# Performance work log

Measured on AMD Instinct MI355X. Metric: run time of the kernel, lower is better.

Reference implementation:

```python
import jax, jax.numpy as jnp
import numpy as np

T, B, D = 1024, 128, 512
CLIP = 1.0  # grad_clip_value


def setup_inputs() -> dict:
    key = jax.random.key(0)
    ks = jax.random.split(key, 6)
    s = 1.0 / np.sqrt(D)
    return {
        "h0": jnp.zeros((B, D), jnp.float32),
        "ins": jax.random.normal(ks[0], (T, B, D), jnp.float32),
        "resets": jax.random.bernoulli(ks[1], 0.05, (T, B)),
        # GRUCell params: input kernels (with bias) for r,z,n fused; hidden kernels
        # for r,z (no bias, per flax GRUCell) fused; hidden kernel for n (with bias).
        "Wi": (jax.random.normal(ks[2], (D, 3 * D), jnp.float32) * s),
        "bi": jnp.zeros((3 * D,), jnp.float32),
        "Wh_rz": (jax.random.normal(ks[3], (D, 2 * D), jnp.float32) * s),
        "Whn": (jax.random.normal(ks[4], (D, D), jnp.float32) * s),
        "bhn": jnp.zeros((D,), jnp.float32),
    }


def reference(h0, ins, resets, Wi, bi, Wh_rz, Whn, bhn):
    def st_clip(x):
        # straight-through clip: forward = clip(x), backward = identity
        return x + jax.lax.stop_gradient(jnp.clip(x, -CLIP, CLIP) - x)

    def step(h, xt):
        x, reset = xt                      # x: [B,D], reset: [B]
        h = jnp.where(reset[:, None], 0.0, h)  # reset carry to zeros
        gi = x @ Wi + bi                   # [B,3D]
        grz = h @ Wh_rz                    # [B,2D]
        r = jax.nn.sigmoid(gi[:, :D] + grz[:, :D])
        z = jax.nn.sigmoid(gi[:, D:2 * D] + grz[:, D:])
        n = jnp.tanh(gi[:, 2 * D:] + r * (h @ Whn + bhn))
        h_new = (1.0 - z) * n + z * h      # GRU update; y == new carry in flax
        h_new = st_clip(h_new)
        return h_new, h_new

    _, ys = jax.lax.scan(step, h0, (ins, resets))
    return ys  # [T,B,D]
```

## Files before the change

kernel.cpp:

```cpp
#include <hip/hip_runtime.h>
#include <stdint.h>


typedef float f32x4 __attribute__((ext_vector_type(4)));
typedef short s16x8 __attribute__((ext_vector_type(8)));

#define DD 512
#define BB 128
#define TT 1024

static __device__ __forceinline__ unsigned short f2bf(float f) {
  uint32_t u = __builtin_bit_cast(uint32_t, f);
  u = (u + 0x7fffu + ((u >> 16) & 1u)) >> 16;
  return (unsigned short)u;
}
static __device__ __forceinline__ float b2f(uint32_t bits) {
  return __builtin_bit_cast(float, bits << 16);
}
static __device__ __forceinline__ s16x8 ldsfrag(const char* p) {
  return __builtin_bit_cast(s16x8, *reinterpret_cast<const uint4*>(p));
}

__global__ void prep(const float* __restrict__ Wi, const float* __restrict__ Whrz,
                     const float* __restrict__ Whn,
                     unsigned short* __restrict__ WiT, unsigned short* __restrict__ Wpk) {
  int i = blockIdx.x * 256 + threadIdx.x;
  if (i < 786432) {
    int n = i >> 9, k = i & 511;
    WiT[i] = f2bf(Wi[(size_t)k * 1536 + n]);
  } else {
    int j = i - 786432;
    int ck = j >> 9;
    int k = j & 511;
    int cj = ck / 96, c96 = ck % 96;
    int g = c96 >> 5, cc = c96 & 31;
    float v = (g < 2) ? Whrz[(size_t)k * 1024 + g * 512 + cj * 32 + cc]
                      : Whn[(size_t)k * 512 + cj * 32 + cc];
    Wpk[j] = f2bf(v);
  }
}

__global__ void tag0(const float* __restrict__ h0, uint32_t* __restrict__ hxt,
                     float* __restrict__ hbF) {
  int i = blockIdx.x * 512 + threadIdx.x;
  float v = h0[i];
  hxt[i] = (uint32_t)f2bf(v);
  hbF[i] = v;
}

__global__ void scanR(const int* __restrict__ r, int* __restrict__ flag) {
  int i = blockIdx.x * 256 + threadIdx.x;
  unsigned int v = (unsigned int)r[i];
  if (v > 1u) atomicOr(flag, 1);
}

__global__ __launch_bounds__(256) void gemmA(const float* __restrict__ x,
                                             const unsigned short* __restrict__ WiT,
                                             const float* __restrict__ bi,
                                             unsigned short* __restrict__ gi) {
  __shared__ unsigned short Al[128 * 64];
  __shared__ unsigned short Bl[128 * 64];
  const int tid = threadIdx.x;
  const int lane = tid & 63;
  const int wv = tid >> 6;
  const int wm = wv >> 1, wn = wv & 1;
  const int n0 = blockIdx.x * 128;
  const int m0 = blockIdx.y * 128;

  const int sr = tid >> 1;
  const int sh = tid & 1;
  const float* xp = x + (size_t)(m0 + sr) * DD + sh * 32;
  const unsigned short* wp = WiT + (size_t)(n0 + sr) * DD + sh * 32;

  float bir[4];
#pragma unroll
  for (int j = 0; j < 4; ++j) bir[j] = bi[n0 + wn * 64 + j * 16 + (lane & 15)];

  f32x4 acc[4][4];
#pragma unroll
  for (int i = 0; i < 4; ++i)
#pragma unroll
    for (int j = 0; j < 4; ++j) acc[i][j] = (f32x4){0.f, 0.f, 0.f, 0.f};

  float4 xa[8];
  uint4 wa[4];
#pragma unroll
  for (int q = 0; q < 8; ++q) xa[q] = *reinterpret_cast<const float4*>(xp + q * 4);
#pragma unroll
  for (int c = 0; c < 4; ++c) wa[c] = *reinterpret_cast<const uint4*>(wp + c * 8);

  for (int kt = 0; kt < 8; ++kt) {
    __syncthreads();
    const int swz = (sr & 7) << 4;
#pragma unroll
    for (int c = 0; c < 4; ++c) {
      const float4 a = xa[2 * c], b = xa[2 * c + 1];
      uint4 u;
      u.x = (uint32_t)f2bf(a.x) | ((uint32_t)f2bf(a.y) << 16);
      u.y = (uint32_t)f2bf(a.z) | ((uint32_t)f2bf(a.w) << 16);
      u.z = (uint32_t)f2bf(b.x) | ((uint32_t)f2bf(b.y) << 16);
      u.w = (uint32_t)f2bf(b.z) | ((uint32_t)f2bf(b.w) << 16);
      const int off = sr * 128 + ((sh * 64 + c * 16) ^ swz);
      *reinterpret_cast<uint4*>(reinterpret_cast<char*>(Al) + off) = u;
    }
#pragma unroll
    for (int c = 0; c < 4; ++c) {
      const int off = sr * 128 + ((sh * 64 + c * 16) ^ swz);
      *reinterpret_cast<uint4*>(reinterpret_cast<char*>(Bl) + off) = wa[c];
    }
    if (kt < 7) {
#pragma unroll
      for (int q = 0; q < 8; ++q)
        xa[q] = *reinterpret_cast<const float4*>(xp + (kt + 1) * 64 + q * 4);
#pragma unroll
      for (int c = 0; c < 4; ++c)
        wa[c] = *reinterpret_cast<const uint4*>(wp + (kt + 1) * 64 + c * 8);
    }
    __syncthreads();
#pragma unroll
    for (int kk = 0; kk < 2; ++kk) {
      s16x8 af[4], bfr[4];
      const int kb = kk * 64 + ((lane >> 4) << 4);
      const int sw = (lane & 7) << 4;
#pragma unroll
      for (int i = 0; i < 4; ++i) {
        const int row = wm * 64 + i * 16 + (lane & 15);
        af[i] = ldsfrag(reinterpret_cast<const char*>(Al) + row * 128 + (kb ^ sw));
      }
#pragma unroll
      for (int j = 0; j < 4; ++j) {
        const int row = wn * 64 + j * 16 + (lane & 15);
        bfr[j] = ldsfrag(reinterpret_cast<const char*>(Bl) + row * 128 + (kb ^ sw));
      }
#pragma unroll
      for (int i = 0; i < 4; ++i)
#pragma unroll
        for (int j = 0; j < 4; ++j)
          acc[i][j] = __builtin_amdgcn_mfma_f32_16x16x32_bf16(af[i], bfr[j], acc[i][j], 0, 0, 0);
    }
  }
#pragma unroll
  for (int i = 0; i < 4; ++i) {
    const int gr0 = m0 + wm * 64 + i * 16 + ((lane >> 4) << 2);
#pragma unroll
    for (int j = 0; j < 4; ++j) {
      const int gc = n0 + wn * 64 + j * 16 + (lane & 15);
#pragma unroll
      for (int r = 0; r < 4; ++r)
        gi[(size_t)(gr0 + r) * 1536 + gc] = f2bf(acc[i][j][r] + bir[j]);
    }
  }
}

static __device__ __forceinline__ unsigned rmask16f(const int* resets, int rmode,
                                                    long long tg, int row0) {
  unsigned m = 0;
  if (rmode) {
    const unsigned char* rb = reinterpret_cast<const unsigned char*>(resets);
    uint4 u = *reinterpret_cast<const uint4*>(rb + (size_t)tg * 128 + row0);
    unsigned w0 = u.x, w1 = u.y, w2 = u.z, w3 = u.w;
#pragma unroll
    for (int b = 0; b < 4; ++b) {
      if ((w0 >> (8 * b)) & 0xFFu) m |= 1u << (0 + b);
      if ((w1 >> (8 * b)) & 0xFFu) m |= 1u << (4 + b);
      if ((w2 >> (8 * b)) & 0xFFu) m |= 1u << (8 + b);
      if ((w3 >> (8 * b)) & 0xFFu) m |= 1u << (12 + b);
    }
  } else {
    const uint4* p = reinterpret_cast<const uint4*>(resets + (size_t)tg * 128 + row0);
#pragma unroll
    for (int q = 0; q < 4; ++q) {
      uint4 u = p[q];
      if (u.x) m |= 1u << (q * 4 + 0);
      if (u.y) m |= 1u << (q * 4 + 1);
      if (u.z) m |= 1u << (q * 4 + 2);
      if (u.w) m |= 1u << (q * 4 + 3);
    }
  }
  return m;
}

static __device__ __forceinline__ void pollTag(const uint32_t* src, unsigned exp,
                                               unsigned short (&v)[16]) {
  for (int it = 0; it < (1 << 16); ++it) {
    uint32_t u[16];
#pragma unroll
    for (int i = 0; i < 16; ++i)
      u[i] = __hip_atomic_load(src + (size_t)i * 512,
                               __ATOMIC_RELAXED, __HIP_MEMORY_SCOPE_AGENT);
    unsigned bad = 0;
#pragma unroll
    for (int i = 0; i < 16; ++i) bad |= ((u[i] >> 16) ^ exp);
    if (__ballot(bad != 0u) == 0ull) {
#pragma unroll
      for (int i = 0; i < 16; ++i) v[i] = (unsigned short)u[i];
      return;
    }
    __builtin_amdgcn_s_sleep(1);
  }
#pragma unroll
  for (int i = 0; i < 16; ++i) v[i] = 0;
}

__global__ __launch_bounds__(512) void rnnB(const unsigned short* __restrict__ gi,
                                            const unsigned short* __restrict__ Wpk,
                                            const float* __restrict__ bhn,
                                            const int* __restrict__ resets,
                                            uint32_t* hxt,
                                            float* hbF,
                                            const int* __restrict__ rmodep,
                                            float* __restrict__ ys,
                                            int t0, int tc) {
  __shared__ char Hlb[16384];
  __shared__ float ax[6528];

  const int tid = threadIdx.x;
  const int lane = tid & 63;
  const int wv = tid >> 6;
  const int w = wv & 1, ks = wv >> 1;
  const int cj = blockIdx.x >> 3, rg = blockIdx.x & 7;
  const int ec = tid & 31, eb = tid >> 5;
  const int bglob = rg * 16 + eb;
  const int colglob = cj * 32 + ec;
  const int rmode = *rmodep;

  uint4 wreg[3][4];
  {
    const unsigned short* wbase = Wpk + (size_t)cj * 96 * 512
                                + (size_t)(w * 16 + (lane & 15)) * 512
                                + ks * 128 + (lane >> 4) * 8;
#pragma unroll
    for (int g = 0; g < 3; ++g)
#pragma unroll
      for (int kk = 0; kk < 4; ++kk)
        wreg[g][kk] = *reinterpret_cast<const uint4*>(wbase + g * 32 * 512 + kk * 32);
  }

  const float bhn_c = bhn[colglob];
  float h_old = hbF[(size_t)bglob * 512 + colglob];

  unsigned short v[16];
  pollTag(hxt + (size_t)(t0 & 1) * 65536 + (size_t)rg * 8192 + tid, (unsigned)t0 & 0xFFFFu, v);

  unsigned mask = rmask16f(resets, rmode, t0, rg * 16);
  uint32_t gir, giz, gin;
  {
    const unsigned short* gp = gi + (size_t)bglob * 1536 + colglob;
    gir = gp[0]; giz = gp[512]; gin = gp[1024];
  }

  int soff[16];
#pragma unroll
  for (int i = 0; i < 16; ++i)
    soff[i] = i * 1024 + (((((tid * 2) >> 4) ^ (i & 7)) << 4) | ((tid & 7) * 2));

  for (int t = 0; t < tc; ++t) {
    const long long tg = t0 + t;
#pragma unroll
    for (int i = 0; i < 16; ++i) {
      unsigned short x = ((mask >> i) & 1u) ? (unsigned short)0 : v[i];
      *reinterpret_cast<unsigned short*>(Hlb + soff[i]) = x;
    }
    __syncthreads();
    f32x4 acc[3];
#pragma unroll
    for (int g = 0; g < 3; ++g) acc[g] = (f32x4){0.f, 0.f, 0.f, 0.f};
    {
      const int rowb = lane & 15;
      const char* hrow = Hlb + rowb * 1024;
      const int hsw = (rowb & 7) << 4;
      const int kplusB = (lane >> 4) << 4;
      s16x8 hfrag[4];
#pragma unroll
      for (int kk = 0; kk < 4; ++kk) {
        const int kbB = (ks * 128 + kk * 32) * 2 + kplusB;
        hfrag[kk] = ldsfrag(hrow + (kbB ^ hsw));
      }
#pragma unroll
      for (int g = 0; g < 3; ++g)
#pragma unroll
        for (int kk = 0; kk < 4; ++kk)
          acc[g] = __builtin_amdgcn_mfma_f32_16x16x32_bf16(
              __builtin_bit_cast(s16x8, wreg[g][kk]), hfrag[kk], acc[g], 0, 0, 0);
    }
    {
      const int mh = (lane >> 4) << 2, nn = lane & 15;
#pragma unroll
      for (int g = 0; g < 3; ++g) {
        float* dst = ax + ((ks * 2 + w) * 3 + g) * 272 + nn;
#pragma unroll
        for (int r = 0; r < 4; ++r) dst[(mh + r) * 17] = acc[g][r];
      }
    }
    __syncthreads();
    {
      const int wc = ec >> 4, mc = ec & 15;
      float s0a = 0.f, s1a = 0.f, s2a = 0.f;
#pragma unroll
      for (int k2 = 0; k2 < 4; ++k2) {
        const float* p = ax + ((k2 * 2 + wc) * 3) * 272 + mc * 17 + eb;
        s0a += p[0]; s1a += p[272]; s2a += p[544];
      }
      const float r = 1.f / (1.f + __expf(-(b2f(gir) + s0a)));
      const float z = 1.f / (1.f + __expf(-(b2f(giz) + s1a)));
      const float hu = ((mask >> eb) & 1u) ? 0.f : h_old;
      const float pre = b2f(gin) + r * (s2a + bhn_c);
      const float n = 1.f - 2.f / (1.f + __expf(2.f * pre));
      float hn = (1.f - z) * n + z * hu;
      hn = fminf(1.f, fmaxf(-1.f, hn));
      __builtin_nontemporal_store(hn, ys + ((size_t)tg * 128 + bglob) * 512 + colglob);
      const uint32_t tagged = (((uint32_t)(tg + 1) & 0xFFFFu) << 16) | (uint32_t)f2bf(hn);
      uint32_t* hp = hxt + (size_t)((tg + 1) & 1) * 65536 + (size_t)bglob * 512 + colglob;
      __hip_atomic_store(hp, tagged, __ATOMIC_RELAXED, __HIP_MEMORY_SCOPE_AGENT);
      if (t == tc - 1) hbF[(size_t)bglob * 512 + colglob] = hn;
      h_old = hn;
    }
    if (t + 1 < tc) {
      const unsigned short* gp = gi + ((size_t)(t + 1) * 128 + bglob) * 1536 + colglob;
      uint32_t ngr = gp[0], ngz = gp[512], ngn = gp[1024];
      unsigned nmask = rmask16f(resets, rmode, tg + 1, rg * 16);
      pollTag(hxt + (size_t)((tg + 1) & 1) * 65536 + (size_t)rg * 8192 + tid,
              (unsigned)(tg + 1) & 0xFFFFu, v);
      gir = ngr; giz = ngz; gin = ngn; mask = nmask;
    }
  }
}

extern "C" void kernel_launch(void* const* d_in, const int* in_sizes, int n_in,
                              void* d_out, int out_size, void* d_ws, size_t ws_size,
                              hipStream_t stream) {
  const float* h0 = (const float*)d_in[0];
  const float* ins = (const float*)d_in[1];
  const int* rst = (const int*)d_in[2];
  const float* Wi = (const float*)d_in[3];
  const float* bi = (const float*)d_in[4];
  const float* Whrz = (const float*)d_in[5];
  const float* Whn = (const float*)d_in[6];
  const float* bhn = (const float*)d_in[7];
  float* ys = (float*)d_out;

  char* ws = (char*)d_ws;
  unsigned short* WiT = (unsigned short*)(ws);
  unsigned short* Wpk = (unsigned short*)(ws + 1572864);
  uint32_t* hxt = (uint32_t*)(ws + 3145728);
  float* hbF = (float*)(ws + 3670016);
  int* flag = (int*)(ws + 3932160);
  const size_t gi_off = 3936256;
  unsigned short* gi = (unsigned short*)(ws + gi_off);

  size_t avail = (ws_size > gi_off) ? (ws_size - gi_off) : 0;
  long long tcap = (long long)(avail / (128ull * 1536ull * 2ull));
  int Tc = (int)((tcap > 1024) ? 1024 : tcap);
  Tc &= ~1;
  if (Tc < 2) Tc = 2;

  hipMemsetAsync(flag, 0, 4, stream);
  hipMemsetAsync(hxt, 0, 524288, stream);
  tag0<<<dim3(128), dim3(512), 0, stream>>>(h0, hxt, hbF);
  prep<<<dim3(6144), dim3(256), 0, stream>>>(Wi, Whrz, Whn, WiT, Wpk);
  scanR<<<dim3(128), dim3(256), 0, stream>>>(rst, flag);

  for (int t0 = 0; t0 < 1024; t0 += Tc) {
    int tc = 1024 - t0;
    if (tc > Tc) tc = Tc;
    gemmA<<<dim3(12, tc), dim3(256), 0, stream>>>(ins + (size_t)t0 * 65536, WiT, bi, gi);
    rnnB<<<dim3(128), dim3(512), 0, stream>>>(gi, Wpk, bhn, rst, hxt, hbF, flag, ys, t0, tc);
  }
}
```

Measured before the change: 3.385 ms.

## Fuse input GEMM and recurrent scan into one persistent producer-consumer kernel

Replaces the separate gemmA launch plus rnnB launch with one kernel of 256 blocks. Blocks 128 and up compute the input-projection tiles and bump a per-timestep done counter, while blocks 0-127 run the recurrence and spin on that counter before reading gi for each step. This lets the large input GEMM overlap with the latency-bound sequential scan instead of running before it. The poll loop also spins without sleeping for its first iterations and has a lower iteration cap. The added risks are deadlock if the producer blocks are not co-resident with the consumers, extra atomic traffic, and the producer blocks contending with the recurrence for CUs and bandwidth.

Result: slower. 9.776 ms (+188.8%).

```diff
diff --git a/kernel.cpp b/kernel.cpp
--- a/kernel.cpp
+++ b/kernel.cpp
@@ -8,6 +8,7 @@
 #define DD 512
 #define BB 128
 #define TT 1024
+#define SM_BYTES 43008
 
 static __device__ __forceinline__ unsigned short f2bf(float f) {
   uint32_t u = __builtin_bit_cast(uint32_t, f);
@@ -54,104 +55,6 @@
   if (v > 1u) atomicOr(flag, 1);
 }
 
-__global__ __launch_bounds__(256) void gemmA(const float* __restrict__ x,
-                                             const unsigned short* __restrict__ WiT,
-                                             const float* __restrict__ bi,
-                                             unsigned short* __restrict__ gi) {
-  __shared__ unsigned short Al[128 * 64];
-  __shared__ unsigned short Bl[128 * 64];
-  const int tid = threadIdx.x;
-  const int lane = tid & 63;
-  const int wv = tid >> 6;
-  const int wm = wv >> 1, wn = wv & 1;
-  const int n0 = blockIdx.x * 128;
-  const int m0 = blockIdx.y * 128;
-
-  const int sr = tid >> 1;
-  const int sh = tid & 1;
-  const float* xp = x + (size_t)(m0 + sr) * DD + sh * 32;
-  const unsigned short* wp = WiT + (size_t)(n0 + sr) * DD + sh * 32;
-
-  float bir[4];
-#pragma unroll
-  for (int j = 0; j < 4; ++j) bir[j] = bi[n0 + wn * 64 + j * 16 + (lane & 15)];
-
-  f32x4 acc[4][4];
-#pragma unroll
-  for (int i = 0; i < 4; ++i)
-#pragma unroll
-    for (int j = 0; j < 4; ++j) acc[i][j] = (f32x4){0.f, 0.f, 0.f, 0.f};
-
-  float4 xa[8];
-  uint4 wa[4];
-#pragma unroll
-  for (int q = 0; q < 8; ++q) xa[q] = *reinterpret_cast<const float4*>(xp + q * 4);
-#pragma unroll
-  for (int c = 0; c < 4; ++c) wa[c] = *reinterpret_cast<const uint4*>(wp + c * 8);
-
-  for (int kt = 0; kt < 8; ++kt) {
-    __syncthreads();
-    const int swz = (sr & 7) << 4;
-#pragma unroll
-    for (int c = 0; c < 4; ++c) {
-      const float4 a = xa[2 * c], b = xa[2 * c + 1];
-      uint4 u;
-      u.x = (uint32_t)f2bf(a.x) | ((uint32_t)f2bf(a.y) << 16);
-      u.y = (uint32_t)f2bf(a.z) | ((uint32_t)f2bf(a.w) << 16);
-      u.z = (uint32_t)f2bf(b.x) | ((uint32_t)f2bf(b.y) << 16);
-      u.w = (uint32_t)f2bf(b.z) | ((uint32_t)f2bf(b.w) << 16);
-      const int off = sr * 128 + ((sh * 64 + c * 16) ^ swz);
-      *reinterpret_cast<uint4*>(reinterpret_cast<char*>(Al) + off) = u;
-    }
-#pragma unroll
-    for (int c = 0; c < 4; ++c) {
-      const int off = sr * 128 + ((sh * 64 + c * 16) ^ swz);
-      *reinterpret_cast<uint4*>(reinterpret_cast<char*>(Bl) + off) = wa[c];
-    }
-    if (kt < 7) {
-#pragma unroll
-      for (int q = 0; q < 8; ++q)
-        xa[q] = *reinterpret_cast<const float4*>(xp + (kt + 1) * 64 + q * 4);
-#pragma unroll
-      for (int c = 0; c < 4; ++c)
-        wa[c] = *reinterpret_cast<const uint4*>(wp + (kt + 1) * 64 + c * 8);
-    }
-    __syncthreads();
-#pragma unroll
-    for (int kk = 0; kk < 2; ++kk) {
-      s16x8 af[4], bfr[4];
-      const int kb = kk * 64 + ((lane >> 4) << 4);
-      const int sw = (lane & 7) << 4;
-#pragma unroll
-      for (int i = 0; i < 4; ++i) {
-        const int row = wm * 64 + i * 16 + (lane & 15);
-        af[i] = ldsfrag(reinterpret_cast<const char*>(Al) + row * 128 + (kb ^ sw));
-      }
-#pragma unroll
-      for (int j = 0; j < 4; ++j) {
-        const int row = wn * 64 + j * 16 + (lane & 15);
-        bfr[j] = ldsfrag(reinterpret_cast<const char*>(Bl) + row * 128 + (kb ^ sw));
-      }
-#pragma unroll
-      for (int i = 0; i < 4; ++i)
-#pragma unroll
-        for (int j = 0; j < 4; ++j)
-          acc[i][j] = __builtin_amdgcn_mfma_f32_16x16x32_bf16(af[i], bfr[j], acc[i][j], 0, 0, 0);
-    }
-  }
-#pragma unroll
-  for (int i = 0; i < 4; ++i) {
-    const int gr0 = m0 + wm * 64 + i * 16 + ((lane >> 4) << 2);
-#pragma unroll
-    for (int j = 0; j < 4; ++j) {
-      const int gc = n0 + wn * 64 + j * 16 + (lane & 15);
-#pragma unroll
-      for (int r = 0; r < 4; ++r)
-        gi[(size_t)(gr0 + r) * 1536 + gc] = f2bf(acc[i][j][r] + bir[j]);
-    }
-  }
-}
-
 static __device__ __forceinline__ unsigned rmask16f(const int* resets, int rmode,
                                                     long long tg, int row0) {
   unsigned m = 0;
@@ -182,7 +85,7 @@
 
 static __device__ __forceinline__ void pollTag(const uint32_t* src, unsigned exp,
                                                unsigned short (&v)[16]) {
-  for (int it = 0; it < (1 << 16); ++it) {
+  for (int it = 0; it < (1 << 13); ++it) {
     uint32_t u[16];
 #pragma unroll
     for (int i = 0; i < 16; ++i)
@@ -196,23 +99,146 @@
       for (int i = 0; i < 16; ++i) v[i] = (unsigned short)u[i];
       return;
     }
-    __builtin_amdgcn_s_sleep(1);
+    if (it >= 2) __builtin_amdgcn_s_sleep(1);
   }
 #pragma unroll
   for (int i = 0; i < 16; ++i) v[i] = 0;
 }
 
-__global__ __launch_bounds__(512) void rnnB(const unsigned short* __restrict__ gi,
-                                            const unsigned short* __restrict__ Wpk,
-                                            const float* __restrict__ bhn,
-                                            const int* __restrict__ resets,
-                                            uint32_t* hxt,
-                                            float* hbF,
-                                            const int* __restrict__ rmodep,
-                                            float* __restrict__ ys,
-                                            int t0, int tc) {
-  __shared__ char Hlb[16384];
-  __shared__ float ax[6528];
+static __device__ __forceinline__ void waitDone(const int* done, int t) {
+  if ((threadIdx.x & 63) == 0) {
+    for (int it = 0; it < (1 << 16); ++it) {
+      if (__hip_atomic_load(done + t, __ATOMIC_ACQUIRE, __HIP_MEMORY_SCOPE_AGENT) >= 12)
+        break;
+      __builtin_amdgcn_s_sleep(2);
+    }
+  }
+}
+
+static __device__ void gemm_role(const float* __restrict__ x,
+                                 const unsigned short* __restrict__ WiT,
+                                 const float* __restrict__ bi,
+                                 uint32_t* __restrict__ gw,
+                                 int* __restrict__ done,
+                                 int tc, int gb, char* smem) {
+  unsigned short* Al = reinterpret_cast<unsigned short*>(smem);
+  unsigned short* Bl = reinterpret_cast<unsigned short*>(smem + 16384);
+  const int tid = threadIdx.x;
+  const int lane = tid & 63;
+  const int wv = tid >> 6;
+  const int wm = wv >> 2, wn = wv & 3;
+  const int sr = tid >> 2;
+  const int sh = tid & 3;
+  const int ntiles = 12 * tc;
+
+  for (int tile = gb; tile < ntiles; tile += 128) {
+    const int tt = tile / 12, nn = tile % 12;
+    const int m0 = tt * 128, n0 = nn * 128;
+    const float* xp = x + (size_t)(m0 + sr) * DD + sh * 16;
+    const unsigned short* wp = WiT + (size_t)(n0 + sr) * DD + sh * 16;
+
+    float bir[2];
+#pragma unroll
+    for (int j = 0; j < 2; ++j) bir[j] = bi[n0 + wn * 32 + j * 16 + (lane & 15)];
+
+    f32x4 acc[4][2];
+#pragma unroll
+    for (int i = 0; i < 4; ++i)
+#pragma unroll
+      for (int j = 0; j < 2; ++j) acc[i][j] = (f32x4){0.f, 0.f, 0.f, 0.f};
+
+    float4 xa[4];
+    uint4 wa[2];
+#pragma unroll
+    for (int q = 0; q < 4; ++q) xa[q] = *reinterpret_cast<const float4*>(xp + q * 4);
+#pragma unroll
+    for (int c = 0; c < 2; ++c) wa[c] = *reinterpret_cast<const uint4*>(wp + c * 8);
+
+    for (int kt = 0; kt < 8; ++kt) {
+      __syncthreads();
+      const int swz = (sr & 7) << 4;
+#pragma unroll
+      for (int c = 0; c < 2; ++c) {
+        const float4 a = xa[2 * c], b = xa[2 * c + 1];
+        uint4 u;
+        u.x = (uint32_t)f2bf(a.x) | ((uint32_t)f2bf(a.y) << 16);
+        u.y = (uint32_t)f2bf(a.z) | ((uint32_t)f2bf(a.w) << 16);
+        u.z = (uint32_t)f2bf(b.x) | ((uint32_t)f2bf(b.y) << 16);
+        u.w = (uint32_t)f2bf(b.z) | ((uint32_t)f2bf(b.w) << 16);
+        const int off = sr * 128 + ((sh * 32 + c * 16) ^ swz);
+        *reinterpret_cast<uint4*>(reinterpret_cast<char*>(Al) + off) = u;
+      }
+#pragma unroll
+      for (int c = 0; c < 2; ++c) {
+        const int off = sr * 128 + ((sh * 32 + c * 16) ^ swz);
+        *reinterpret_cast<uint4*>(reinterpret_cast<char*>(Bl) + off) = wa[c];
+      }
+      if (kt < 7) {
+#pragma unroll
+        for (int q = 0; q < 4; ++q)
+          xa[q] = *reinterpret_cast<const float4*>(xp + (kt + 1) * 64 + q * 4);
+#pragma unroll
+        for (int c = 0; c < 2; ++c)
+          wa[c] = *reinterpret_cast<const uint4*>(wp + (kt + 1) * 64 + c * 8);
+      }
+      __syncthreads();
+#pragma unroll
+      for (int kk = 0; kk < 2; ++kk) {
+        s16x8 af[4], bfr[2];
+        const int kb = kk * 64 + ((lane >> 4) << 4);
+        const int sw = (lane & 7) << 4;
+#pragma unroll
+        for (int i = 0; i < 4; ++i) {
+          const int row = wm * 64 + i * 16 + (lane & 15);
+          af[i] = ldsfrag(reinterpret_cast<const char*>(Al) + row * 128 + (kb ^ sw));
+        }
+#pragma unroll
+        for (int j = 0; j < 2; ++j) {
+          const int row = wn * 32 + j * 16 + (lane & 15);
+          bfr[j] = ldsfrag(reinterpret_cast<const char*>(Bl) + row * 128 + (kb ^ sw));
+        }
+#pragma unroll
+        for (int i = 0; i < 4; ++i)
+#pragma unroll
+          for (int j = 0; j < 2; ++j)
+            acc[i][j] = __builtin_amdgcn_mfma_f32_16x16x32_bf16(af[i], bfr[j], acc[i][j], 0, 0, 0);
+      }
+    }
+#pragma unroll
+    for (int i = 0; i < 4; ++i) {
+      const int row0 = m0 + wm * 64 + i * 16 + ((lane >> 4) << 2);
+#pragma unroll
+      for (int j = 0; j < 2; ++j) {
+        const int col = n0 + wn * 32 + j * 16 + (lane & 15);
+#pragma unroll
+        for (int r = 0; r < 4; ++r) {
+          float s = acc[i][j][r] + bir[j];
+          unsigned myb = f2bf(s);
+          unsigned hib = (unsigned)__shfl_down((int)myb, 1) & 0xFFFFu;
+          if (!(lane & 1)) {
+            uint32_t word = myb | (hib << 16);
+            __hip_atomic_store(gw + (size_t)(row0 + r) * 768 + (col >> 1), word,
+                               __ATOMIC_RELAXED, __HIP_MEMORY_SCOPE_AGENT);
+          }
+        }
+      }
+    }
+    __syncthreads();
+    if (tid == 0)
+      __hip_atomic_fetch_add(done + tt, 1, __ATOMIC_RELEASE, __HIP_MEMORY_SCOPE_AGENT);
+  }
+}
+
+static __device__ void rnn_role(const uint32_t* __restrict__ gw,
+                                const unsigned short* __restrict__ Wpk,
+                                const float* __restrict__ bhn,
+                                const int* __restrict__ resets,
+                                uint32_t* hxt, float* hbF,
+                                int rmode, const int* __restrict__ done,
+                                float* __restrict__ ys,
+                                int t0, int tc, char* smem) {
+  char* Hlb = smem;
+  float* ax = reinterpret_cast<float*>(smem + 16384);
 
   const int tid = threadIdx.x;
   const int lane = tid & 63;
@@ -222,7 +248,7 @@
   const int ec = tid & 31, eb = tid >> 5;
   const int bglob = rg * 16 + eb;
   const int colglob = cj * 32 + ec;
-  const int rmode = *rmodep;
+  const int gsh = (colglob & 1) << 4;
 
   uint4 wreg[3][4];
   {
@@ -245,8 +271,12 @@
   unsigned mask = rmask16f(resets, rmode, t0, rg * 16);
   uint32_t gir, giz, gin;
   {
-    const unsigned short* gp = gi + (size_t)bglob * 1536 + colglob;
-    gir = gp[0]; giz = gp[512]; gin = gp[1024];
+    waitDone(done, 0);
+    const uint32_t* gp = gw + (size_t)bglob * 768 + (colglob >> 1);
+    uint32_t wr = __hip_atomic_load(gp, __ATOMIC_RELAXED, __HIP_MEMORY_SCOPE_AGENT);
+    uint32_t wz = __hip_atomic_load(gp + 256, __ATOMIC_RELAXED, __HIP_MEMORY_SCOPE_AGENT);
+    uint32_t wn_ = __hip_atomic_load(gp + 512, __ATOMIC_RELAXED, __HIP_MEMORY_SCOPE_AGENT);
+    gir = (wr >> gsh) & 0xFFFFu; giz = (wz >> gsh) & 0xFFFFu; gin = (wn_ >> gsh) & 0xFFFFu;
   }
 
   int soff[16];
@@ -284,10 +314,10 @@
               __builtin_bit_cast(s16x8, wreg[g][kk]), hfrag[kk], acc[g], 0, 0, 0);
     }
     {
-      const int mh = (lane >> 4) << 2, nn = lane & 15;
+      const int mh = (lane >> 4) << 2, nnn = lane & 15;
 #pragma unroll
       for (int g = 0; g < 3; ++g) {
-        float* dst = ax + ((ks * 2 + w) * 3 + g) * 272 + nn;
+        float* dst = ax + ((ks * 2 + w) * 3 + g) * 272 + nnn;
 #pragma unroll
         for (int r = 0; r < 4; ++r) dst[(mh + r) * 17] = acc[g][r];
       }
@@ -310,20 +340,44 @@
       hn = fminf(1.f, fmaxf(-1.f, hn));
       __builtin_nontemporal_store(hn, ys + ((size_t)tg * 128 + bglob) * 512 + colglob);
       const uint32_t tagged = (((uint32_t)(tg + 1) & 0xFFFFu) << 16) | (uint32_t)f2bf(hn);
-      uint32_t* hp = hxt + (size_t)((tg + 1) & 1) * 65536 + (size_t)bglob * 512 + colglob;
-      __hip_atomic_store(hp, tagged, __ATOMIC_RELAXED, __HIP_MEMORY_SCOPE_AGENT);
+      __hip_atomic_store(hxt + (size_t)((tg + 1) & 1) * 65536 + (size_t)bglob * 512 + colglob,
+                         tagged, __ATOMIC_RELAXED, __HIP_MEMORY_SCOPE_AGENT);
       if (t == tc - 1) hbF[(size_t)bglob * 512 + colglob] = hn;
       h_old = hn;
     }
     if (t + 1 < tc) {
-      const unsigned short* gp = gi + ((size_t)(t + 1) * 128 + bglob) * 1536 + colglob;
-      uint32_t ngr = gp[0], ngz = gp[512], ngn = gp[1024];
+      waitDone(done, t + 1);
+      const uint32_t* gp = gw + ((size_t)(t + 1) * 128 + bglob) * 768 + (colglob >> 1);
+      uint32_t wr = __hip_atomic_load(gp, __ATOMIC_RELAXED, __HIP_MEMORY_SCOPE_AGENT);
+      uint32_t wz = __hip_atomic_load(gp + 256, __ATOMIC_RELAXED, __HIP_MEMORY_SCOPE_AGENT);
+      uint32_t wn_ = __hip_atomic_load(gp + 512, __ATOMIC_RELAXED, __HIP_MEMORY_SCOPE_AGENT);
       unsigned nmask = rmask16f(resets, rmode, tg + 1, rg * 16);
       pollTag(hxt + (size_t)((tg + 1) & 1) * 65536 + (size_t)rg * 8192 + tid,
               (unsigned)(tg + 1) & 0xFFFFu, v);
-      gir = ngr; giz = ngz; gin = ngn; mask = nmask;
-    }
-  }
+      gir = (wr >> gsh) & 0xFFFFu; giz = (wz >> gsh) & 0xFFFFu; gin = (wn_ >> gsh) & 0xFFFFu;
+      mask = nmask;
+    }
+  }
+}
+
+__global__ __launch_bounds__(512) void fused(const float* __restrict__ x,
+                                             const unsigned short* __restrict__ WiT,
+                                             const float* __restrict__ bi,
+                                             uint32_t* gw,
+                                             const unsigned short* __restrict__ Wpk,
+                                             const float* __restrict__ bhn,
+                                             const int* __restrict__ resets,
+                                             uint32_t* hxt, float* hbF,
+                                             const int* __restrict__ rmodep,
+                                             int* done,
+                                             float* __restrict__ ys,
+                                             int t0, int tc) {
+  __shared__ char smem[SM_BYTES];
+  if (blockIdx.x >= 128) {
+    gemm_role(x, WiT, bi, gw, done, tc, blockIdx.x - 128, smem);
+    return;
+  }
+  rnn_role(gw, Wpk, bhn, resets, hxt, hbF, *rmodep, done, ys, t0, tc, smem);
 }
 
 extern "C" void kernel_launch(void* const* d_in, const int* in_sizes, int n_in,
@@ -345,8 +399,9 @@
   uint32_t* hxt = (uint32_t*)(ws + 3145728);
   float* hbF = (float*)(ws + 3670016);
   int* flag = (int*)(ws + 3932160);
-  const size_t gi_off = 3936256;
-  unsigned short* gi = (unsigned short*)(ws + gi_off);
+  int* done = (int*)(ws + 3936256);
+  const size_t gi_off = 3940352;
+  uint32_t* gw = (uint32_t*)(ws + gi_off);
 
   size_t avail = (ws_size > gi_off) ? (ws_size - gi_off) : 0;
   long long tcap = (long long)(avail / (128ull * 1536ull * 2ull));
@@ -363,7 +418,9 @@
   for (int t0 = 0; t0 < 1024; t0 += Tc) {
     int tc = 1024 - t0;
     if (tc > Tc) tc = Tc;
-    gemmA<<<dim3(12, tc), dim3(256), 0, stream>>>(ins + (size_t)t0 * 65536, WiT, bi, gi);
-    rnnB<<<dim3(128), dim3(512), 0, stream>>>(gi, Wpk, bhn, rst, hxt, hbF, flag, ys, t0, tc);
-  }
-}
+    hipMemsetAsync(done, 0, (size_t)tc * 4, stream);
+    fused<<<dim3(256), dim3(512), 0, stream>>>(ins + (size_t)t0 * 65536, WiT, bi, gw,
+                                               Wpk, bhn, rst, hxt, hbF, flag, done, ys,
+                                               t0, tc);
+  }
+}
```

## Fuse input projection GEMM into persistent recurrent kernel

Applied to the files above, without the earlier changes.

Removes the separate gemmA pass that precomputed x@Wi into a bf16 workspace. The persistent rnnB kernel now holds both the input and hidden weight slices in registers, prefetches the next x rows, and does the input-projection MFMAs inside each timestep. The aim is to drop the large intermediate write/read and the chunked relaunches. The cost is more MFMA work on the serial critical path and higher register and LDS pressure. Polling was also reworked to a per-lane done flag with a wave-wide ballot exit and a lower iteration cap.

Result: slower. 3.516 ms (+3.9%).

```diff
diff --git a/kernel.cpp b/kernel.cpp
--- a/kernel.cpp
+++ b/kernel.cpp
@@ -23,15 +23,16 @@
 
 __global__ void prep(const float* __restrict__ Wi, const float* __restrict__ Whrz,
                      const float* __restrict__ Whn,
-                     unsigned short* __restrict__ WiT, unsigned short* __restrict__ Wpk) {
+                     unsigned short* __restrict__ Wipk, unsigned short* __restrict__ Wpk) {
   int i = blockIdx.x * 256 + threadIdx.x;
   if (i < 786432) {
-    int n = i >> 9, k = i & 511;
-    WiT[i] = f2bf(Wi[(size_t)k * 1536 + n]);
+    int ck = i >> 9, k = i & 511;
+    int cj = ck / 96, c96 = ck % 96;
+    int g = c96 >> 5, cc = c96 & 31;
+    Wipk[i] = f2bf(Wi[(size_t)k * 1536 + g * 512 + cj * 32 + cc]);
   } else {
     int j = i - 786432;
-    int ck = j >> 9;
-    int k = j & 511;
+    int ck = j >> 9, k = j & 511;
     int cj = ck / 96, c96 = ck % 96;
     int g = c96 >> 5, cc = c96 & 31;
     float v = (g < 2) ? Whrz[(size_t)k * 1024 + g * 512 + cj * 32 + cc]
@@ -52,104 +53,6 @@
   int i = blockIdx.x * 256 + threadIdx.x;
   unsigned int v = (unsigned int)r[i];
   if (v > 1u) atomicOr(flag, 1);
-}
-
-__global__ __launch_bounds__(256) void gemmA(const float* __restrict__ x,
-                                             const unsigned short* __restrict__ WiT,
-                                             const float* __restrict__ bi,
-                                             unsigned short* __restrict__ gi) {
-  __shared__ unsigned short Al[128 * 64];
-  __shared__ unsigned short Bl[128 * 64];
-  const int tid = threadIdx.x;
-  const int lane = tid & 63;
-  const int wv = tid >> 6;
-  const int wm = wv >> 1, wn = wv & 1;
-  const int n0 = blockIdx.x * 128;
-  const int m0 = blockIdx.y * 128;
-
-  const int sr = tid >> 1;
-  const int sh = tid & 1;
-  const float* xp = x + (size_t)(m0 + sr) * DD + sh * 32;
-  const unsigned short* wp = WiT + (size_t)(n0 + sr) * DD + sh * 32;
-
-  float bir[4];
-#pragma unroll
-  for (int j = 0; j < 4; ++j) bir[j] = bi[n0 + wn * 64 + j * 16 + (lane & 15)];
-
-  f32x4 acc[4][4];
-#pragma unroll
-  for (int i = 0; i < 4; ++i)
-#pragma unroll
-    for (int j = 0; j < 4; ++j) acc[i][j] = (f32x4){0.f, 0.f, 0.f, 0.f};
-
-  float4 xa[8];
-  uint4 wa[4];
-#pragma unroll
-  for (int q = 0; q < 8; ++q) xa[q] = *reinterpret_cast<const float4*>(xp + q * 4);
-#pragma unroll
-  for (int c = 0; c < 4; ++c) wa[c] = *reinterpret_cast<const uint4*>(wp + c * 8);
-
-  for (int kt = 0; kt < 8; ++kt) {
-    __syncthreads();
-    const int swz = (sr & 7) << 4;
-#pragma unroll
-    for (int c = 0; c < 4; ++c) {
-      const float4 a = xa[2 * c], b = xa[2 * c + 1];
-      uint4 u;
-      u.x = (uint32_t)f2bf(a.x) | ((uint32_t)f2bf(a.y) << 16);
-      u.y = (uint32_t)f2bf(a.z) | ((uint32_t)f2bf(a.w) << 16);
-      u.z = (uint32_t)f2bf(b.x) | ((uint32_t)f2bf(b.y) << 16);
-      u.w = (uint32_t)f2bf(b.z) | ((uint32_t)f2bf(b.w) << 16);
-      const int off = sr * 128 + ((sh * 64 + c * 16) ^ swz);
-      *reinterpret_cast<uint4*>(reinterpret_cast<char*>(Al) + off) = u;
-    }
-#pragma unroll
-    for (int c = 0; c < 4; ++c) {
-      const int off = sr * 128 + ((sh * 64 + c * 16) ^ swz);
-      *reinterpret_cast<uint4*>(reinterpret_cast<char*>(Bl) + off) = wa[c];
-    }
-    if (kt < 7) {
-#pragma unroll
-      for (int q = 0; q < 8; ++q)
-        xa[q] = *reinterpret_cast<const float4*>(xp + (kt + 1) * 64 + q * 4);
-#pragma unroll
-      for (int c = 0; c < 4; ++c)
-        wa[c] = *reinterpret_cast<const uint4*>(wp + (kt + 1) * 64 + c * 8);
-    }
-    __syncthreads();
-#pragma unroll
-    for (int kk = 0; kk < 2; ++kk) {
-      s16x8 af[4], bfr[4];
-      const int kb = kk * 64 + ((lane >> 4) << 4);
-      const int sw = (lane & 7) << 4;
-#pragma unroll
-      for (int i = 0; i < 4; ++i) {
-        const int row = wm * 64 + i * 16 + (lane & 15);
-        af[i] = ldsfrag(reinterpret_cast<const char*>(Al) + row * 128 + (kb ^ sw));
-      }
-#pragma unroll
-      for (int j = 0; j < 4; ++j) {
-        const int row = wn * 64 + j * 16 + (lane & 15);
-        bfr[j] = ldsfrag(reinterpret_cast<const char*>(Bl) + row * 128 + (kb ^ sw));
-      }
-#pragma unroll
-      for (int i = 0; i < 4; ++i)
-#pragma unroll
-        for (int j = 0; j < 4; ++j)
-          acc[i][j] = __builtin_amdgcn_mfma_f32_16x16x32_bf16(af[i], bfr[j], acc[i][j], 0, 0, 0);
-    }
-  }
-#pragma unroll
-  for (int i = 0; i < 4; ++i) {
-    const int gr0 = m0 + wm * 64 + i * 16 + ((lane >> 4) << 2);
-#pragma unroll
-    for (int j = 0; j < 4; ++j) {
-      const int gc = n0 + wn * 64 + j * 16 + (lane & 15);
-#pragma unroll
-      for (int r = 0; r < 4; ++r)
-        gi[(size_t)(gr0 + r) * 1536 + gc] = f2bf(acc[i][j][r] + bir[j]);
-    }
-  }
 }
 
 static __device__ __forceinline__ unsigned rmask16f(const int* resets, int rmode,
@@ -182,37 +85,45 @@
 
 static __device__ __forceinline__ void pollTag(const uint32_t* src, unsigned exp,
                                                unsigned short (&v)[16]) {
-  for (int it = 0; it < (1 << 16); ++it) {
-    uint32_t u[16];
-#pragma unroll
-    for (int i = 0; i < 16; ++i)
-      u[i] = __hip_atomic_load(src + (size_t)i * 512,
-                               __ATOMIC_RELAXED, __HIP_MEMORY_SCOPE_AGENT);
-    unsigned bad = 0;
-#pragma unroll
-    for (int i = 0; i < 16; ++i) bad |= ((u[i] >> 16) ^ exp);
-    if (__ballot(bad != 0u) == 0ull) {
-#pragma unroll
-      for (int i = 0; i < 16; ++i) v[i] = (unsigned short)u[i];
-      return;
-    }
-    __builtin_amdgcn_s_sleep(1);
-  }
-#pragma unroll
-  for (int i = 0; i < 16; ++i) v[i] = 0;
-}
-
-__global__ __launch_bounds__(512) void rnnB(const unsigned short* __restrict__ gi,
+  bool need = true;
+  for (int it = 0; it < (1 << 12); ++it) {
+    if (need) {
+      uint32_t u[16];
+#pragma unroll
+      for (int i = 0; i < 16; ++i)
+        u[i] = __hip_atomic_load(src + (size_t)i * 512,
+                                 __ATOMIC_RELAXED, __HIP_MEMORY_SCOPE_AGENT);
+      unsigned bad = 0;
+#pragma unroll
+      for (int i = 0; i < 16; ++i) bad |= ((u[i] >> 16) ^ exp);
+      if (bad == 0u) {
+#pragma unroll
+        for (int i = 0; i < 16; ++i) v[i] = (unsigned short)u[i];
+        need = false;
+      }
+    }
+    if (__ballot(need ? 1 : 0) == 0ull) break;
+    if (it >= 1) __builtin_amdgcn_s_sleep(1);
+  }
+}
+
+#define RNN_SMEM (16384 + 16384 + 34816)
+
+__global__ __launch_bounds__(512) void rnnB(const float* __restrict__ x,
+                                            const unsigned short* __restrict__ Wipk,
                                             const unsigned short* __restrict__ Wpk,
+                                            const float* __restrict__ bi,
                                             const float* __restrict__ bhn,
                                             const int* __restrict__ resets,
                                             uint32_t* hxt,
-                                            float* hbF,
+                                            const float* __restrict__ hbF,
                                             const int* __restrict__ rmodep,
                                             float* __restrict__ ys,
-                                            int t0, int tc) {
-  __shared__ char Hlb[16384];
-  __shared__ float ax[6528];
+                                            int tc) {
+  extern __shared__ char smem[];
+  char* Hlb = smem;
+  char* Xlb = smem + 16384;
+  float* ax = reinterpret_cast<float*>(smem + 32768);
 
   const int tid = threadIdx.x;
   const int lane = tid & 63;
@@ -224,30 +135,34 @@
   const int colglob = cj * 32 + ec;
   const int rmode = *rmodep;
 
-  uint4 wreg[3][4];
+  uint4 wreg[3][4], wireg[3][4];
   {
-    const unsigned short* wbase = Wpk + (size_t)cj * 96 * 512
-                                + (size_t)(w * 16 + (lane & 15)) * 512
-                                + ks * 128 + (lane >> 4) * 8;
+    const size_t fb = (size_t)cj * 96 * 512
+                    + (size_t)(w * 16 + (lane & 15)) * 512
+                    + ks * 128 + (lane >> 4) * 8;
 #pragma unroll
     for (int g = 0; g < 3; ++g)
 #pragma unroll
-      for (int kk = 0; kk < 4; ++kk)
-        wreg[g][kk] = *reinterpret_cast<const uint4*>(wbase + g * 32 * 512 + kk * 32);
+      for (int kk = 0; kk < 4; ++kk) {
+        wreg[g][kk]  = *reinterpret_cast<const uint4*>(Wpk  + fb + g * 32 * 512 + kk * 32);
+        wireg[g][kk] = *reinterpret_cast<const uint4*>(Wipk + fb + g * 32 * 512 + kk * 32);
+      }
   }
 
   const float bhn_c = bhn[colglob];
+  float bir3[3];
+#pragma unroll
+  for (int g = 0; g < 3; ++g) bir3[g] = bi[g * 512 + colglob];
   float h_old = hbF[(size_t)bglob * 512 + colglob];
 
   unsigned short v[16];
-  pollTag(hxt + (size_t)(t0 & 1) * 65536 + (size_t)rg * 8192 + tid, (unsigned)t0 & 0xFFFFu, v);
-
-  unsigned mask = rmask16f(resets, rmode, t0, rg * 16);
-  uint32_t gir, giz, gin;
-  {
-    const unsigned short* gp = gi + (size_t)bglob * 1536 + colglob;
-    gir = gp[0]; giz = gp[512]; gin = gp[1024];
-  }
+  pollTag(hxt + (size_t)rg * 8192 + tid, 0u, v);
+  unsigned mask = rmask16f(resets, rmode, 0, rg * 16);
+
+  float xa[16];
+#pragma unroll
+  for (int i = 0; i < 16; ++i)
+    xa[i] = x[(size_t)(rg * 16 + i) * 512 + tid];
 
   int soff[16];
 #pragma unroll
@@ -255,73 +170,89 @@
     soff[i] = i * 1024 + (((((tid * 2) >> 4) ^ (i & 7)) << 4) | ((tid & 7) * 2));
 
   for (int t = 0; t < tc; ++t) {
-    const long long tg = t0 + t;
+    float xaN[16];
+    const bool haveN = (t + 1 < tc);
+    if (haveN) {
+#pragma unroll
+      for (int i = 0; i < 16; ++i)
+        xaN[i] = x[((size_t)(t + 1) * 128 + rg * 16 + i) * 512 + tid];
+    }
 #pragma unroll
     for (int i = 0; i < 16; ++i) {
-      unsigned short x = ((mask >> i) & 1u) ? (unsigned short)0 : v[i];
-      *reinterpret_cast<unsigned short*>(Hlb + soff[i]) = x;
+      unsigned short hv = ((mask >> i) & 1u) ? (unsigned short)0 : v[i];
+      *reinterpret_cast<unsigned short*>(Hlb + soff[i]) = hv;
+      *reinterpret_cast<unsigned short*>(Xlb + soff[i]) = f2bf(xa[i]);
     }
     __syncthreads();
-    f32x4 acc[3];
-#pragma unroll
-    for (int g = 0; g < 3; ++g) acc[g] = (f32x4){0.f, 0.f, 0.f, 0.f};
+    f32x4 accR = (f32x4){0.f, 0.f, 0.f, 0.f};
+    f32x4 accZ = accR, accNX = accR, accNH = accR;
     {
       const int rowb = lane & 15;
-      const char* hrow = Hlb + rowb * 1024;
       const int hsw = (rowb & 7) << 4;
       const int kplusB = (lane >> 4) << 4;
-      s16x8 hfrag[4];
+      s16x8 hfrag[4], xfrag[4];
 #pragma unroll
       for (int kk = 0; kk < 4; ++kk) {
         const int kbB = (ks * 128 + kk * 32) * 2 + kplusB;
-        hfrag[kk] = ldsfrag(hrow + (kbB ^ hsw));
-      }
-#pragma unroll
-      for (int g = 0; g < 3; ++g)
-#pragma unroll
-        for (int kk = 0; kk < 4; ++kk)
-          acc[g] = __builtin_amdgcn_mfma_f32_16x16x32_bf16(
-              __builtin_bit_cast(s16x8, wreg[g][kk]), hfrag[kk], acc[g], 0, 0, 0);
+        hfrag[kk] = ldsfrag(Hlb + rowb * 1024 + (kbB ^ hsw));
+        xfrag[kk] = ldsfrag(Xlb + rowb * 1024 + (kbB ^ hsw));
+      }
+#pragma unroll
+      for (int kk = 0; kk < 4; ++kk) {
+        accR = __builtin_amdgcn_mfma_f32_16x16x32_bf16(
+            __builtin_bit_cast(s16x8, wireg[0][kk]), xfrag[kk], accR, 0, 0, 0);
+        accZ = __builtin_amdgcn_mfma_f32_16x16x32_bf16(
+            __builtin_bit_cast(s16x8, wireg[1][kk]), xfrag[kk], accZ, 0, 0, 0);
+        accNX = __builtin_amdgcn_mfma_f32_16x16x32_bf16(
+            __builtin_bit_cast(s16x8, wireg[2][kk]), xfrag[kk], accNX, 0, 0, 0);
+        accR = __builtin_amdgcn_mfma_f32_16x16x32_bf16(
+            __builtin_bit_cast(s16x8, wreg[0][kk]), hfrag[kk], accR, 0, 0, 0);
+        accZ = __builtin_amdgcn_mfma_f32_16x16x32_bf16(
+            __builtin_bit_cast(s16x8, wreg[1][kk]), hfrag[kk], accZ, 0, 0, 0);
+        accNH = __builtin_amdgcn_mfma_f32_16x16x32_bf16(
+            __builtin_bit_cast(s16x8, wreg[2][kk]), hfrag[kk], accNH, 0, 0, 0);
+      }
     }
     {
       const int mh = (lane >> 4) << 2, nn = lane & 15;
-#pragma unroll
-      for (int g = 0; g < 3; ++g) {
-        float* dst = ax + ((ks * 2 + w) * 3 + g) * 272 + nn;
-#pragma unroll
-        for (int r = 0; r < 4; ++r) dst[(mh + r) * 17] = acc[g][r];
+      float* base = ax + (size_t)((ks * 2 + w) * 4) * 272 + nn;
+#pragma unroll
+      for (int r = 0; r < 4; ++r) {
+        base[(mh + r) * 17] = accR[r];
+        base[272 + (mh + r) * 17] = accZ[r];
+        base[544 + (mh + r) * 17] = accNX[r];
+        base[816 + (mh + r) * 17] = accNH[r];
       }
     }
     __syncthreads();
     {
       const int wc = ec >> 4, mc = ec & 15;
-      float s0a = 0.f, s1a = 0.f, s2a = 0.f;
+      float s0 = 0.f, s1 = 0.f, s2x = 0.f, s2h = 0.f;
 #pragma unroll
       for (int k2 = 0; k2 < 4; ++k2) {
-        const float* p = ax + ((k2 * 2 + wc) * 3) * 272 + mc * 17 + eb;
-        s0a += p[0]; s1a += p[272]; s2a += p[544];
-      }
-      const float r = 1.f / (1.f + __expf(-(b2f(gir) + s0a)));
-      const float z = 1.f / (1.f + __expf(-(b2f(giz) + s1a)));
+        const float* p = ax + (size_t)((k2 * 2 + wc) * 4) * 272 + mc * 17 + eb;
+        s0 += p[0]; s1 += p[272]; s2x += p[544]; s2h += p[816];
+      }
+      const float r = 1.f / (1.f + __expf(-(bir3[0] + s0)));
+      const float z = 1.f / (1.f + __expf(-(bir3[1] + s1)));
       const float hu = ((mask >> eb) & 1u) ? 0.f : h_old;
-      const float pre = b2f(gin) + r * (s2a + bhn_c);
+      const float pre = (bir3[2] + s2x) + r * (s2h + bhn_c);
       const float n = 1.f - 2.f / (1.f + __expf(2.f * pre));
       float hn = (1.f - z) * n + z * hu;
       hn = fminf(1.f, fmaxf(-1.f, hn));
-      __builtin_nontemporal_store(hn, ys + ((size_t)tg * 128 + bglob) * 512 + colglob);
-      const uint32_t tagged = (((uint32_t)(tg + 1) & 0xFFFFu) << 16) | (uint32_t)f2bf(hn);
-      uint32_t* hp = hxt + (size_t)((tg + 1) & 1) * 65536 + (size_t)bglob * 512 + colglob;
-      __hip_atomic_store(hp, tagged, __ATOMIC_RELAXED, __HIP_MEMORY_SCOPE_AGENT);
-      if (t == tc - 1) hbF[(size_t)bglob * 512 + colglob] = hn;
+      const uint32_t tagged = (((uint32_t)(t + 1) & 0xFFFFu) << 16) | (uint32_t)f2bf(hn);
+      __hip_atomic_store(hxt + (size_t)((t + 1) & 1) * 65536 + (size_t)bglob * 512 + colglob,
+                         tagged, __ATOMIC_RELAXED, __HIP_MEMORY_SCOPE_AGENT);
+      __builtin_nontemporal_store(hn, ys + ((size_t)t * 128 + bglob) * 512 + colglob);
       h_old = hn;
     }
-    if (t + 1 < tc) {
-      const unsigned short* gp = gi + ((size_t)(t + 1) * 128 + bglob) * 1536 + colglob;
-      uint32_t ngr = gp[0], ngz = gp[512], ngn = gp[1024];
-      unsigned nmask = rmask16f(resets, rmode, tg + 1, rg * 16);
-      pollTag(hxt + (size_t)((tg + 1) & 1) * 65536 + (size_t)rg * 8192 + tid,
-              (unsigned)(tg + 1) & 0xFFFFu, v);
-      gir = ngr; giz = ngz; gin = ngn; mask = nmask;
+    if (haveN) {
+      unsigned nmask = rmask16f(resets, rmode, t + 1, rg * 16);
+      pollTag(hxt + (size_t)((t + 1) & 1) * 65536 + (size_t)rg * 8192 + tid,
+              (unsigned)(t + 1) & 0xFFFFu, v);
+      mask = nmask;
+#pragma unroll
+      for (int i = 0; i < 16; ++i) xa[i] = xaN[i];
     }
   }
 }
@@ -340,30 +271,19 @@
   float* ys = (float*)d_out;
 
   char* ws = (char*)d_ws;
-  unsigned short* WiT = (unsigned short*)(ws);
-  unsigned short* Wpk = (unsigned short*)(ws + 1572864);
+  unsigned short* Wpk = (unsigned short*)(ws);
+  unsigned short* Wipk = (unsigned short*)(ws + 1572864);
   uint32_t* hxt = (uint32_t*)(ws + 3145728);
   float* hbF = (float*)(ws + 3670016);
   int* flag = (int*)(ws + 3932160);
-  const size_t gi_off = 3936256;
-  unsigned short* gi = (unsigned short*)(ws + gi_off);
-
-  size_t avail = (ws_size > gi_off) ? (ws_size - gi_off) : 0;
-  long long tcap = (long long)(avail / (128ull * 1536ull * 2ull));
-  int Tc = (int)((tcap > 1024) ? 1024 : tcap);
-  Tc &= ~1;
-  if (Tc < 2) Tc = 2;
 
   hipMemsetAsync(flag, 0, 4, stream);
   hipMemsetAsync(hxt, 0, 524288, stream);
   tag0<<<dim3(128), dim3(512), 0, stream>>>(h0, hxt, hbF);
-  prep<<<dim3(6144), dim3(256), 0, stream>>>(Wi, Whrz, Whn, WiT, Wpk);
+  prep<<<dim3(6144), dim3(256), 0, stream>>>(Wi, Whrz, Whn, Wipk, Wpk);
   scanR<<<dim3(128), dim3(256), 0, stream>>>(rst, flag);
-
-  for (int t0 = 0; t0 < 1024; t0 += Tc) {
-    int tc = 1024 - t0;
-    if (tc > Tc) tc = Tc;
-    gemmA<<<dim3(12, tc), dim3(256), 0, stream>>>(ins + (size_t)t0 * 65536, WiT, bi, gi);
-    rnnB<<<dim3(128), dim3(512), 0, stream>>>(gi, Wpk, bhn, rst, hxt, hbF, flag, ys, t0, tc);
-  }
-}
+  hipFuncSetAttribute((const void*)rnnB, hipFuncAttributeMaxDynamicSharedMemorySize,
+                      RNN_SMEM);
+  rnnB<<<dim3(128), dim3(512), RNN_SMEM, stream>>>(ins, Wipk, Wpk, bi, bhn, rst,
+                                                   hxt, hbF, flag, ys, 1024);
+}
```
